# Performance work log

Hardware: AMD Instinct MI355X
Metric: run time of the kernel (lower is better)

The kernel has to match this reference:

```python
import jax, jax.numpy as jnp
import numpy as np

S, LC = 4096, 16
N_WORD, N_CHAR = 100000, 128
CHAR_DIM, CHAR_HIDDEN = 64, 128
N_DIM, N_HIDDEN, N_TAG = 256, 512, 64


def setup_inputs() -> dict:
    key = jax.random.key(0)
    ks = jax.random.split(key, 16)
    rn = lambda k, shape, s=0.1: (jax.random.normal(k, shape, jnp.float32) * s)
    inp = {
        'char_emb': rn(ks[0], (N_CHAR, CHAR_DIM), 1.0),
        'char_Wih': rn(ks[1], (4 * CHAR_HIDDEN, CHAR_DIM)),
        'char_Whh': rn(ks[2], (4 * CHAR_HIDDEN, CHAR_HIDDEN)),
        'char_bih': rn(ks[3], (4 * CHAR_HIDDEN,)),
        'char_bhh': rn(ks[4], (4 * CHAR_HIDDEN,)),
        'word_emb': rn(ks[5], (N_WORD, N_DIM), 1.0),
        'Wih': rn(ks[6], (4 * N_HIDDEN, N_DIM + CHAR_HIDDEN)),
        'Whh': rn(ks[7], (4 * N_HIDDEN, N_HIDDEN)),
        'bih': rn(ks[8], (4 * N_HIDDEN,)),
        'bhh': rn(ks[9], (4 * N_HIDDEN,)),
        'W1': rn(ks[10], (N_TAG, N_HIDDEN)),
        'b1': rn(ks[11], (N_TAG,)),
        'x': jax.random.randint(ks[12], (S,), 0, N_WORD),
        'chars': jax.random.randint(ks[13], (S, LC), 0, N_CHAR),
        'char_lens': jax.random.randint(ks[14], (S,), 1, LC + 1),
    }
    return inp


def _lstm(xs, mask, Wih, Whh, bih, bhh):
    # xs: [T, B, In], mask: [T, B] bool. PyTorch gate order: i, f, g, o.
    T, B, _ = xs.shape
    H = Whh.shape[1]
    def step(carry, inp):
        h, c = carry
        x_t, m_t = inp
        g = x_t @ Wih.T + bih + h @ Whh.T + bhh  # [B, 4H]
        i, f, gg, o = jnp.split(g, 4, axis=-1)
        c_new = jax.nn.sigmoid(f) * c + jax.nn.sigmoid(i) * jnp.tanh(gg)
        h_new = jax.nn.sigmoid(o) * jnp.tanh(c_new)
        m = m_t[:, None]
        h2 = jnp.where(m, h_new, h)
        c2 = jnp.where(m, c_new, c)
        return (h2, c2), h2
    init = (jnp.zeros((B, H), xs.dtype), jnp.zeros((B, H), xs.dtype))
    (h_fin, _), hs = jax.lax.scan(step, init, (xs, mask))
    return hs, h_fin


def reference(char_emb, char_Wih, char_Whh, char_bih, char_bhh,
              word_emb, Wih, Whh, bih, bhh, W1, b1,
              x, chars, char_lens):
    # --- char-level LSTM, all S words batched (replaces per-word Python loop) ---
    cx = char_emb[chars]                      # [S, LC, char_dim]
    cx = jnp.transpose(cx, (1, 0, 2))         # [LC, S, char_dim]
    cmask = jnp.arange(LC)[:, None] < char_lens[None, :]  # [LC, S]
    _, char_h = _lstm(cx, cmask, char_Wih, char_Whh, char_bih, char_bhh)  # [S, char_hidden]

    # --- word-level LSTM over the sentence (batch 1, as in original) ---
    wx = word_emb[x]                          # [S, n_dim]
    feat = jnp.concatenate([wx, char_h], axis=-1)[:, None, :]  # [S, 1, n_dim+char_hidden]
    wmask = jnp.ones((feat.shape[0], 1), bool)
    hs, _ = _lstm(feat, wmask, Wih, Whh, bih, bhh)  # [S, 1, n_hidden]
    hs = hs[:, 0, :]

    logits = hs @ W1.T + b1                   # [S, n_tag]
    return jax.nn.log_softmax(logits, axis=-1)
```

## Files before the change

### kernel.cpp

```cpp
#include <hip/hip_runtime.h>
#include <hip/hip_bf16.h>


#define OFF_FLAG  0
#define OFF_CEMB  16
#define OFF_CWIH  8208
#define OFF_CBIH  40976
#define OFF_CBHH  41488
#define OFF_CWHH  42000
#define OFF_BIH   107536
#define OFF_BHH   109584
#define OFF_W1T   111632
#define OFF_CGE   144400
#define OFF_CH    209936
#define OFF_XP2   734224
#define OFF_HH    4928528

#define SENT 0xFFFFFFFFu

__device__ __forceinline__ float sigf(float x) { return 1.0f / (1.0f + __expf(-x)); }
__device__ __forceinline__ float tanh_f(float x) { return 2.0f * sigf(2.0f * x) - 1.0f; }
__device__ __forceinline__ float b2f_lo(unsigned u) { return __uint_as_float(u << 16); }
__device__ __forceinline__ float b2f_hi(unsigned u) { return __uint_as_float(u & 0xFFFF0000u); }

__global__ void detect_kernel(const unsigned* __restrict__ w, int* __restrict__ flagp) {
    unsigned v = w[threadIdx.x];
    unsigned e = (v >> 7) & 0xFF;
    int inr = (e >= 100 && e <= 140) ? 1 : 0;
    unsigned long long m = __ballot(inr);
    if (threadIdx.x == 0) flagp[0] = (__popcll(m) >= 56) ? 1 : 0;
}

__global__ void convf_kernel(const void* __restrict__ s, float* __restrict__ d,
                             int n, const int* __restrict__ flagp) {
    int i = blockIdx.x * 256 + threadIdx.x;
    if (i >= n) return;
    d[i] = flagp[0] ? __bfloat162float(((const __hip_bfloat16*)s)[i])
                    : ((const float*)s)[i];
}

__global__ void w1t_kernel(const void* __restrict__ W1, float* __restrict__ W1T,
                           const int* __restrict__ flagp) {
    int i = blockIdx.x * 256 + threadIdx.x;
    int j = i & 63, k = i >> 6;
    W1T[i] = flagp[0] ? __bfloat162float(((const __hip_bfloat16*)W1)[j * 512 + k])
                      : ((const float*)W1)[j * 512 + k];
}

__global__ void __launch_bounds__(256) cge_kernel(
    const float* __restrict__ cemb, const float* __restrict__ cWih,
    const float* __restrict__ cbih, const float* __restrict__ cbhh,
    float* __restrict__ cge)
{
    __shared__ float xe[64];
    int c = blockIdx.x, tid = threadIdx.x;
    if (tid < 64) xe[tid] = cemb[c * 64 + tid];
    __syncthreads();
#pragma unroll
    for (int rep = 0; rep < 2; ++rep) {
        int j = rep * 256 + tid;
        float acc = cbih[j] + cbhh[j];
#pragma unroll 8
        for (int k = 0; k < 64; ++k)
            acc += xe[k] * cWih[j * 64 + k];
        cge[c * 512 + j] = acc;
    }
}

__global__ void __launch_bounds__(256) char_lstm_kernel(
    const float* __restrict__ cge, const float* __restrict__ Whh,
    const int* __restrict__ chars, const int* __restrict__ lens,
    float* __restrict__ char_h)
{
    __shared__ float hls[16][128];
    int tid = threadIdx.x;
    int wl = tid >> 4, sl = tid & 15;
    int w = blockIdx.x * 16 + wl;
    int len = lens[w];
    const int* cw = chars + w * 16;
    float c[8];
#pragma unroll
    for (int q = 0; q < 8; ++q) { c[q] = 0.0f; hls[wl][sl * 8 + q] = 0.0f; }

    for (int t = 0; t < 16; ++t) {
        __syncthreads();
        int ch = cw[t];
        const float* xg = cge + ch * 512;
        float acc[4][8];
#pragma unroll
        for (int g = 0; g < 4; ++g)
#pragma unroll
            for (int q = 0; q < 8; ++q)
                acc[g][q] = xg[g * 128 + sl * 8 + q];

        const float4* h4 = (const float4*)hls[wl];
#pragma unroll
        for (int g = 0; g < 4; ++g) {
            const float4* wbase = ((const float4*)Whh) + (g * 128 + sl * 8) * 32;
            for (int k4 = 0; k4 < 32; ++k4) {
                float4 hv = h4[k4];
#pragma unroll
                for (int q = 0; q < 8; ++q) {
                    float4 wv = wbase[q * 32 + k4];
                    acc[g][q] += wv.x * hv.x + wv.y * hv.y + wv.z * hv.z + wv.w * hv.w;
                }
            }
        }
        __syncthreads();
        if (t < len) {
#pragma unroll
            for (int q = 0; q < 8; ++q) {
                float iv = sigf(acc[0][q]);
                float fv = sigf(acc[1][q]);
                float gv = tanh_f(acc[2][q]);
                float ov = sigf(acc[3][q]);
                c[q] = fv * c[q] + iv * gv;
                hls[wl][sl * 8 + q] = ov * tanh_f(c[q]);
            }
        }
    }
    __syncthreads();
#pragma unroll
    for (int q = 0; q < 8; ++q)
        char_h[w * 128 + sl * 8 + q] = hls[wl][sl * 8 + q];
}

__global__ void __launch_bounds__(256) xp2_kernel(
    const void* __restrict__ wemb, const int* __restrict__ x,
    const float* __restrict__ char_h, const void* __restrict__ Wraw,
    const float* __restrict__ bih, const float* __restrict__ bhh,
    __hip_bfloat16* __restrict__ xp2, const int* __restrict__ flagp)
{
    __shared__ float feat[16][384];
    int flag = flagp[0];
    int tid = threadIdx.x, tl = tid >> 4, sl = tid & 15;
    int t = blockIdx.x * 16 + tl;
    int xw = x[t];
    for (int idx = sl; idx < 384; idx += 16) {
        float v;
        if (idx < 256)
            v = flag ? __bfloat162float(((const __hip_bfloat16*)wemb)[(size_t)xw * 256 + idx])
                     : ((const float*)wemb)[(size_t)xw * 256 + idx];
        else
            v = char_h[t * 128 + (idx - 256)];
        feat[tl][idx] = v;
    }
    __syncthreads();

    const float4* f4 = (const float4*)feat[tl];
    for (int rb = 0; rb < 4; ++rb) {
        int r0 = rb * 512 + sl * 32;
        for (int qc = 0; qc < 4; ++qc) {
            int rr = r0 + qc * 8;
            float acc[8];
#pragma unroll
            for (int q = 0; q < 8; ++q)
                acc[q] = bih[rr + q] + bhh[rr + q];
            if (!flag) {
                const float4* wb = ((const float4*)Wraw) + (size_t)rr * 96;
                for (int k4 = 0; k4 < 96; ++k4) {
                    float4 fv = f4[k4];
#pragma unroll
                    for (int q = 0; q < 8; ++q) {
                        float4 wv = wb[q * 96 + k4];
                        acc[q] += wv.x * fv.x + wv.y * fv.y + wv.z * fv.z + wv.w * fv.w;
                    }
                }
            } else {
                const uint2* wb = ((const uint2*)Wraw) + (size_t)rr * 96;
                for (int k4 = 0; k4 < 96; ++k4) {
                    float4 fv = f4[k4];
#pragma unroll
                    for (int q = 0; q < 8; ++q) {
                        uint2 wv = wb[q * 96 + k4];
                        acc[q] += b2f_lo(wv.x) * fv.x + b2f_hi(wv.x) * fv.y
                                + b2f_lo(wv.y) * fv.z + b2f_hi(wv.y) * fv.w;
                    }
                }
            }
#pragma unroll
            for (int q = 0; q < 8; ++q)
                xp2[(size_t)t * 2048 + rr + q] = __float2bfloat16(acc[q]);
        }
    }
}

__global__ void __launch_bounds__(1024, 4) word_lstm_kernel(
    const __hip_bfloat16* __restrict__ xp2, const void* __restrict__ Whh_raw,
    float* __restrict__ h_hist, const int* __restrict__ flagp)
{
    __shared__ float hpad[2][576];
    __shared__ float hout[16];
    __shared__ int step_flag;
    int flag = flagp[0];
    int wg = blockIdx.x;
    int tid = threadIdx.x;
    int wave = tid >> 6, lane = tid & 63;
    int g = lane >> 4, kk = lane & 15;
    int slot = wg * 16 + wave;
    int grow = g * 512 + slot;

    float4 wreg[8];
    if (!flag) {
        const float4* wr = (const float4*)((const float*)Whh_raw + (size_t)grow * 512 + kk * 32);
#pragma unroll
        for (int i = 0; i < 8; ++i) wreg[i] = wr[i];
    } else {
        const uint2* wr = (const uint2*)((const unsigned short*)Whh_raw + (size_t)grow * 512 + kk * 32);
#pragma unroll
        for (int i = 0; i < 8; ++i) {
            uint2 u = wr[i];
            wreg[i] = make_float4(b2f_lo(u.x), b2f_hi(u.x), b2f_lo(u.y), b2f_hi(u.y));
        }
    }

    for (int i = tid; i < 576; i += 1024) hpad[0][i] = 0.0f;
    if (tid == 0) step_flag = 0;
    __syncthreads();

    unsigned* hview = (unsigned*)h_hist;
    float c = 0.0f;

    for (int t = 0; t < 4096; ++t) {
        float xv = __bfloat162float(xp2[(size_t)t * 2048 + grow]);

        unsigned ls = 0;
        while (__hip_atomic_load(&step_flag, __ATOMIC_ACQUIRE,
                                 __HIP_MEMORY_SCOPE_WORKGROUP) < t) {
            if (++ls > (1u << 24)) break;
        }

        const float4* h4 = (const float4*)(&hpad[t & 1][kk * 36]);
        float acc = 0.0f;
#pragma unroll
        for (int i = 0; i < 8; ++i) {
            float4 hv = h4[i];
            acc += wreg[i].x * hv.x + wreg[i].y * hv.y +
                   wreg[i].z * hv.z + wreg[i].w * hv.w;
        }
        acc += __shfl_xor(acc, 1);
        acc += __shfl_xor(acc, 2);
        acc += __shfl_xor(acc, 4);
        acc += __shfl_xor(acc, 8);
        float gvt = acc + xv;

        float iv = __shfl(gvt, kk);
        float fv = __shfl(gvt, 16 + kk);
        float gg = __shfl(gvt, 32 + kk);
        float ov = __shfl(gvt, 48 + kk);
        c = sigf(fv) * c + sigf(iv) * tanh_f(gg);
        float h = sigf(ov) * tanh_f(c);

        if (lane == 0) hout[wave] = h;
        __syncthreads();

        if (wave == 0) {
            if (lane < 16)
                __hip_atomic_store(hview + (size_t)t * 512 + wg * 16 + lane,
                                   __float_as_uint(hout[lane]),
                                   __ATOMIC_RELAXED, __HIP_MEMORY_SCOPE_AGENT);

            if (t < 4095) {
                unsigned v[8];
                if ((lane >> 1) == wg) {
#pragma unroll
                    for (int i = 0; i < 8; ++i)
                        v[i] = __float_as_uint(hout[(lane & 1) * 8 + i]);
                } else {
                    const unsigned* src = hview + (size_t)t * 512 + lane * 8;
                    unsigned spins = 0;
                    bool bail = false;
                    for (;;) {
#pragma unroll
                        for (int i = 0; i < 8; ++i)
                            v[i] = __hip_atomic_load(src + i, __ATOMIC_RELAXED,
                                                     __HIP_MEMORY_SCOPE_AGENT);
                        int ok = 1;
#pragma unroll
                        for (int i = 0; i < 8; ++i) ok &= (v[i] != SENT);
                        if (ok) break;
                        if (++spins > (1u << 22)) { bail = true; break; }
                    }
                    if (bail) {
#pragma unroll
                        for (int i = 0; i < 8; ++i) v[i] = __float_as_uint(12345.0f);
                    }
                }
                float* dst = &hpad[(t + 1) & 1][(lane >> 2) * 36 + (lane & 3) * 8];
                ((float4*)dst)[0] = make_float4(__uint_as_float(v[0]), __uint_as_float(v[1]),
                                                __uint_as_float(v[2]), __uint_as_float(v[3]));
                ((float4*)dst)[1] = make_float4(__uint_as_float(v[4]), __uint_as_float(v[5]),
                                                __uint_as_float(v[6]), __uint_as_float(v[7]));
                __hip_atomic_store(&step_flag, t + 1, __ATOMIC_RELEASE,
                                   __HIP_MEMORY_SCOPE_WORKGROUP);
            }
        }
    }
}

__global__ void __launch_bounds__(64) out_kernel(
    const float* __restrict__ h_hist, const float* __restrict__ W1T,
    const void* __restrict__ b1raw, void* __restrict__ out,
    const int* __restrict__ flagp)
{
    __shared__ float hb[512];
    int flag = flagp[0];
    int t = blockIdx.x, j = threadIdx.x;
    const float4* src = (const float4*)(h_hist + (size_t)t * 512);
    ((float4*)hb)[j * 2] = src[j * 2];
    ((float4*)hb)[j * 2 + 1] = src[j * 2 + 1];
    __syncthreads();

    float acc = flag ? __bfloat162float(((const __hip_bfloat16*)b1raw)[j])
                     : ((const float*)b1raw)[j];
#pragma unroll 8
    for (int k = 0; k < 512; ++k)
        acc += hb[k] * W1T[k * 64 + j];

    float m = acc;
#pragma unroll
    for (int o = 32; o; o >>= 1) m = fmaxf(m, __shfl_xor(m, o));
    float e = __expf(acc - m);
    float s = e;
#pragma unroll
    for (int o = 32; o; o >>= 1) s += __shfl_xor(s, o);
    float r = acc - m - __logf(s);
    if (flag) ((__hip_bfloat16*)out)[t * 64 + j] = __float2bfloat16(r);
    else      ((float*)out)[t * 64 + j] = r;
}

extern "C" void kernel_launch(void* const* d_in, const int* in_sizes, int n_in,
                              void* d_out, int out_size, void* d_ws, size_t ws_size,
                              hipStream_t stream)
{
    (void)in_sizes; (void)n_in; (void)out_size; (void)ws_size;
    const void* char_emb = d_in[0];
    const void* char_Wih = d_in[1];
    const void* char_Whh = d_in[2];
    const void* char_bih = d_in[3];
    const void* char_bhh = d_in[4];
    const void* word_emb = d_in[5];
    const void* Wih      = d_in[6];
    const void* Whh      = d_in[7];
    const void* bih      = d_in[8];
    const void* bhh      = d_in[9];
    const void* W1       = d_in[10];
    const void* b1       = d_in[11];
    const int* x     = (const int*)d_in[12];
    const int* chars = (const int*)d_in[13];
    const int* lens  = (const int*)d_in[14];

    float* ws    = (float*)d_ws;
    int*   flagp = (int*)(ws + OFF_FLAG);
    float* cembf = ws + OFF_CEMB;
    float* cWihf = ws + OFF_CWIH;
    float* cbihf = ws + OFF_CBIH;
    float* cbhhf = ws + OFF_CBHH;
    float* cWhhf = ws + OFF_CWHH;
    float* bihf  = ws + OFF_BIH;
    float* bhhf  = ws + OFF_BHH;
    float* W1T   = ws + OFF_W1T;
    float* cge   = ws + OFF_CGE;
    float* charh = ws + OFF_CH;
    __hip_bfloat16* xp2 = (__hip_bfloat16*)(ws + OFF_XP2);
    float* hh    = ws + OFF_HH;

    hipMemsetAsync(hh, 0xFF, (size_t)4096 * 512 * 4, stream);

    detect_kernel<<<1, 64, 0, stream>>>((const unsigned*)char_emb, flagp);

    convf_kernel<<<(8192 + 255) / 256, 256, 0, stream>>>(char_emb, cembf, 8192, flagp);
    convf_kernel<<<(32768 + 255) / 256, 256, 0, stream>>>(char_Wih, cWihf, 32768, flagp);
    convf_kernel<<<2, 256, 0, stream>>>(char_bih, cbihf, 512, flagp);
    convf_kernel<<<2, 256, 0, stream>>>(char_bhh, cbhhf, 512, flagp);
    convf_kernel<<<(65536 + 255) / 256, 256, 0, stream>>>(char_Whh, cWhhf, 65536, flagp);
    convf_kernel<<<8, 256, 0, stream>>>(bih, bihf, 2048, flagp);
    convf_kernel<<<8, 256, 0, stream>>>(bhh, bhhf, 2048, flagp);
    w1t_kernel<<<128, 256, 0, stream>>>(W1, W1T, flagp);

    cge_kernel<<<128, 256, 0, stream>>>(cembf, cWihf, cbihf, cbhhf, cge);
    char_lstm_kernel<<<256, 256, 0, stream>>>(cge, cWhhf, chars, lens, charh);
    xp2_kernel<<<256, 256, 0, stream>>>(word_emb, x, charh, Wih, bihf, bhhf, xp2, flagp);
    word_lstm_kernel<<<32, 1024, 0, stream>>>(xp2, Whh, hh, flagp);
    out_kernel<<<4096, 64, 0, stream>>>(hh, W1T, b1, d_out, flagp);
}
```

Before: 13.51 ms.

## Halve word-LSTM workgroups and let every wave poll global h directly

The persistent word-level LSTM kernel now runs on 16 workgroups instead of 32. Each wave handles two hidden units (32 lanes per unit, 8 lanes per gate row, 64 weights per lane held in registers). The old scheme had wave 0 gather h from global memory and release a shared-memory step flag to the other waves. Now each wave spins on the global h history itself and copies it into its own private LDS buffer, which removes the intra-workgroup flag handoff from the critical path. The cost is more global polling traffic per step, double the register weights per lane, and fewer CUs taking part in the recurrence.

```diff
diff --git a/kernel.cpp b/kernel.cpp
--- a/kernel.cpp
+++ b/kernel.cpp
@@ -189,112 +189,103 @@
     const __hip_bfloat16* __restrict__ xp2, const void* __restrict__ Whh_raw,
     float* __restrict__ h_hist, const int* __restrict__ flagp)
 {
-    __shared__ float hpad[2][576];
-    __shared__ float hout[16];
-    __shared__ int step_flag;
+    __shared__ float hbuf[16][576];
+    __shared__ float hout[32];
     int flag = flagp[0];
     int wg = blockIdx.x;
     int tid = threadIdx.x;
     int wave = tid >> 6, lane = tid & 63;
-    int g = lane >> 4, kk = lane & 15;
-    int slot = wg * 16 + wave;
+    int sp = lane >> 5;
+    int g  = (lane >> 3) & 3;
+    int kk = lane & 7;
+    int slot = wg * 32 + wave * 2 + sp;
     int grow = g * 512 + slot;
 
-    float4 wreg[8];
+    float4 wreg[16];
     if (!flag) {
-        const float4* wr = (const float4*)((const float*)Whh_raw + (size_t)grow * 512 + kk * 32);
-#pragma unroll
-        for (int i = 0; i < 8; ++i) wreg[i] = wr[i];
+        const float4* wr = (const float4*)((const float*)Whh_raw + (size_t)grow * 512 + kk * 64);
+#pragma unroll
+        for (int i = 0; i < 16; ++i) wreg[i] = wr[i];
     } else {
-        const uint2* wr = (const uint2*)((const unsigned short*)Whh_raw + (size_t)grow * 512 + kk * 32);
-#pragma unroll
-        for (int i = 0; i < 8; ++i) {
+        const uint2* wr = (const uint2*)((const unsigned short*)Whh_raw + (size_t)grow * 512 + kk * 64);
+#pragma unroll
+        for (int i = 0; i < 16; ++i) {
             uint2 u = wr[i];
             wreg[i] = make_float4(b2f_lo(u.x), b2f_hi(u.x), b2f_lo(u.y), b2f_hi(u.y));
         }
     }
 
-    for (int i = tid; i < 576; i += 1024) hpad[0][i] = 0.0f;
-    if (tid == 0) step_flag = 0;
-    __syncthreads();
-
     unsigned* hview = (unsigned*)h_hist;
+    float* wbuf = hbuf[wave];
     float c = 0.0f;
+    int dead = 0;
 
     for (int t = 0; t < 4096; ++t) {
         float xv = __bfloat162float(xp2[(size_t)t * 2048 + grow]);
 
-        unsigned ls = 0;
-        while (__hip_atomic_load(&step_flag, __ATOMIC_ACQUIRE,
-                                 __HIP_MEMORY_SCOPE_WORKGROUP) < t) {
-            if (++ls > (1u << 24)) break;
-        }
-
-        const float4* h4 = (const float4*)(&hpad[t & 1][kk * 36]);
+        if (t == 0) {
+#pragma unroll
+            for (int i = 0; i < 8; ++i)
+                wbuf[(2 * i + (lane >> 5)) * 36 + (lane & 31)] = 0.0f;
+        } else {
+            const unsigned* src = hview + (size_t)(t - 1) * 512 + lane;
+            unsigned v[8];
+            unsigned spins = 0;
+            for (;;) {
+#pragma unroll
+                for (int i = 0; i < 8; ++i)
+                    v[i] = __hip_atomic_load(src + (size_t)i * 64, __ATOMIC_RELAXED,
+                                             __HIP_MEMORY_SCOPE_AGENT);
+                int ok = 1;
+#pragma unroll
+                for (int i = 0; i < 8; ++i) ok &= (v[i] != SENT);
+                if (dead || __all(ok)) break;
+                if (++spins > (1u << 20)) { dead = 1; break; }
+            }
+            if (dead) {
+#pragma unroll
+                for (int i = 0; i < 8; ++i)
+                    if (v[i] == SENT) v[i] = __float_as_uint(12345.0f);
+            }
+#pragma unroll
+            for (int i = 0; i < 8; ++i)
+                wbuf[(2 * i + (lane >> 5)) * 36 + (lane & 31)] = __uint_as_float(v[i]);
+        }
+
+        const float4* p0 = (const float4*)(wbuf + kk * 72);
+        const float4* p1 = (const float4*)(wbuf + kk * 72 + 36);
         float acc = 0.0f;
 #pragma unroll
         for (int i = 0; i < 8; ++i) {
-            float4 hv = h4[i];
+            float4 hv = p0[i];
             acc += wreg[i].x * hv.x + wreg[i].y * hv.y +
                    wreg[i].z * hv.z + wreg[i].w * hv.w;
+        }
+#pragma unroll
+        for (int i = 0; i < 8; ++i) {
+            float4 hv = p1[i];
+            acc += wreg[8 + i].x * hv.x + wreg[8 + i].y * hv.y +
+                   wreg[8 + i].z * hv.z + wreg[8 + i].w * hv.w;
         }
         acc += __shfl_xor(acc, 1);
         acc += __shfl_xor(acc, 2);
         acc += __shfl_xor(acc, 4);
-        acc += __shfl_xor(acc, 8);
         float gvt = acc + xv;
 
-        float iv = __shfl(gvt, kk);
-        float fv = __shfl(gvt, 16 + kk);
-        float gg = __shfl(gvt, 32 + kk);
-        float ov = __shfl(gvt, 48 + kk);
+        float iv = __shfl(gvt, sp * 32 + 0);
+        float fv = __shfl(gvt, sp * 32 + 8);
+        float gg = __shfl(gvt, sp * 32 + 16);
+        float ov = __shfl(gvt, sp * 32 + 24);
         c = sigf(fv) * c + sigf(iv) * tanh_f(gg);
         float h = sigf(ov) * tanh_f(c);
 
-        if (lane == 0) hout[wave] = h;
+        if ((lane & 31) == 0) hout[wave * 2 + sp] = h;
         __syncthreads();
 
-        if (wave == 0) {
-            if (lane < 16)
-                __hip_atomic_store(hview + (size_t)t * 512 + wg * 16 + lane,
-                                   __float_as_uint(hout[lane]),
-                                   __ATOMIC_RELAXED, __HIP_MEMORY_SCOPE_AGENT);
-
-            if (t < 4095) {
-                unsigned v[8];
-                if ((lane >> 1) == wg) {
-#pragma unroll
-                    for (int i = 0; i < 8; ++i)
-                        v[i] = __float_as_uint(hout[(lane & 1) * 8 + i]);
-                } else {
-                    const unsigned* src = hview + (size_t)t * 512 + lane * 8;
-                    unsigned spins = 0;
-                    bool bail = false;
-                    for (;;) {
-#pragma unroll
-                        for (int i = 0; i < 8; ++i)
-                            v[i] = __hip_atomic_load(src + i, __ATOMIC_RELAXED,
-                                                     __HIP_MEMORY_SCOPE_AGENT);
-                        int ok = 1;
-#pragma unroll
-                        for (int i = 0; i < 8; ++i) ok &= (v[i] != SENT);
-                        if (ok) break;
-                        if (++spins > (1u << 22)) { bail = true; break; }
-                    }
-                    if (bail) {
-#pragma unroll
-                        for (int i = 0; i < 8; ++i) v[i] = __float_as_uint(12345.0f);
-                    }
-                }
-                float* dst = &hpad[(t + 1) & 1][(lane >> 2) * 36 + (lane & 3) * 8];
-                ((float4*)dst)[0] = make_float4(__uint_as_float(v[0]), __uint_as_float(v[1]),
-                                                __uint_as_float(v[2]), __uint_as_float(v[3]));
-                ((float4*)dst)[1] = make_float4(__uint_as_float(v[4]), __uint_as_float(v[5]),
-                                                __uint_as_float(v[6]), __uint_as_float(v[7]));
-                __hip_atomic_store(&step_flag, t + 1, __ATOMIC_RELEASE,
-                                   __HIP_MEMORY_SCOPE_WORKGROUP);
-            }
-        }
+        if (wave == 0 && lane < 32)
+            __hip_atomic_store(hview + (size_t)t * 512 + wg * 32 + lane,
+                               __float_as_uint(hout[lane]),
+                               __ATOMIC_RELAXED, __HIP_MEMORY_SCOPE_AGENT);
     }
 }
 
@@ -381,6 +372,6 @@
     cge_kernel<<<128, 256, 0, stream>>>(cembf, cWihf, cbihf, cbhhf, cge);
     char_lstm_kernel<<<256, 256, 0, stream>>>(cge, cWhhf, chars, lens, charh);
     xp2_kernel<<<256, 256, 0, stream>>>(word_emb, x, charh, Wih, bihf, bhhf, xp2, flagp);
-    word_lstm_kernel<<<32, 1024, 0, stream>>>(xp2, Whh, hh, flagp);
+    word_lstm_kernel<<<16, 1024, 0, stream>>>(xp2, Whh, hh, flagp);
     out_kernel<<<4096, 64, 0, stream>>>(hh, W1T, b1, d_out, flagp);
 }
```

After: 12.64 ms. -6.4%, faster.
